# Performance work log

Measured on AMD Instinct MI355X. Metric: run time of the kernel, lower is better.

Reference implementation:

```python
import jax, jax.numpy as jnp
import numpy as np


def _dct_mats(N):
    # torch_dct.dct with norm=None: X_k = 2 * sum_n x_n cos(pi*(2n+1)k/(2N))
    # torch_dct.idct with norm=None is its exact inverse:
    #   x_n = (1/N) * (X_0/2 + sum_{k>=1} X_k cos(pi*(2n+1)k/(2N)))
    n = np.arange(N)
    k = np.arange(N)
    ang = np.pi * (2 * n[None, :] + 1) * k[:, None] / (2 * N)  # [k, n]
    cosang = np.cos(ang)
    D = (2.0 * cosang).astype(np.float32)                      # [k, n] DCT-II matrix
    scale = np.where(k == 0, 0.5, 1.0) / N                     # k=0 halved, /N overall
    Dinv = (cosang.T * scale[None, :]).astype(np.float32)      # [n, k] inverse matrix
    return jnp.asarray(D), jnp.asarray(Dinv)


def setup_inputs() -> dict:
    key = jax.random.key(0)
    k1, k2 = jax.random.split(key)
    B, C, H, W = 16, 28, 256, 256
    x = jax.random.normal(k1, (B, C, H, W), dtype=jnp.float32)
    weight = jax.random.normal(k2, (H, W, C), dtype=jnp.float32) * 0.02
    return {"x": x, "weight": weight}


def reference(x, weight):
    B, C, H, W = x.shape
    D, Dinv = _dct_mats(C)
    xt = jnp.transpose(x, (0, 2, 3, 1))            # [B, H, W, C]
    xd = jnp.einsum('bhwn,kn->bhwk', xt, D)        # DCT-II along channel dim
    xd = xd * weight                               # per-pixel spectral filter
    out = jnp.einsum('bhwk,nk->bhwn', xd, Dinv)    # inverse DCT along channel dim
    return jnp.transpose(out, (0, 3, 1, 2))        # back to [B, C, H, W]
```

## Files before the change

### kernel.cpp

```cpp
#include <hip/hip_runtime.h>

#define C_DIM 28
#define HW 65536
#define B_DIM 16

namespace {

constexpr double K_PI = 3.14159265358979323846;

constexpr double cos_taylor(double u) {
    double u2 = u * u;
    double term = 1.0, sum = 1.0;
    for (int i = 1; i <= 12; ++i) {
        term *= -u2 / (double)((2 * i - 1) * (2 * i));
        sum += term;
    }
    return sum;
}

constexpr double cos_pi_over56(int t) {
    t %= 112;
    if (t < 0) t += 112;
    double sign = 1.0;
    if (t > 56) t = 112 - t;
    if (t > 28) { t = 56 - t; sign = -1.0; }
    return sign * cos_taylor(K_PI * (double)t / 56.0);
}

struct Tables {
    float D[C_DIM][C_DIM];
    float Dinv[C_DIM][C_DIM];
};

constexpr Tables make_tables() {
    Tables t{};
    for (int k = 0; k < C_DIM; ++k) {
        for (int n = 0; n < C_DIM; ++n) {
            double c = cos_pi_over56((2 * n + 1) * k);
            t.D[k][n]    = (float)(2.0 * c);
            t.Dinv[n][k] = (float)(c * ((k == 0) ? 0.5 : 1.0) / (double)C_DIM);
        }
    }
    return t;
}

constexpr Tables TBL = make_tables();

}

__global__ __launch_bounds__(256) void spedct_kernel(
    const float* __restrict__ x,
    const float* __restrict__ w,
    float* __restrict__ out) {

    const int p  = blockIdx.x * 256 + threadIdx.x;
    const int b  = p >> 16;
    const int hw = p & 0xFFFF;

    const float* xp = x + (size_t)b * (C_DIM * HW) + hw;

    float xv[C_DIM];
#pragma unroll
    for (int n = 0; n < C_DIM; ++n) xv[n] = xp[(size_t)n * HW];

    float wv[C_DIM];
    const float4* wp = (const float4*)(w + (size_t)hw * C_DIM);
#pragma unroll
    for (int i = 0; i < 7; ++i) {
        float4 v = wp[i];
        wv[4 * i + 0] = v.x; wv[4 * i + 1] = v.y;
        wv[4 * i + 2] = v.z; wv[4 * i + 3] = v.w;
    }

    float xd[C_DIM];
#pragma unroll
    for (int k = 0; k < C_DIM; ++k) xd[k] = 0.0f;
#pragma unroll
    for (int n = 0; n < C_DIM; ++n) {
        const float xn = xv[n];
#pragma unroll
        for (int k = 0; k < C_DIM; ++k)
            xd[k] = fmaf(TBL.D[k][n], xn, xd[k]);
    }

#pragma unroll
    for (int k = 0; k < C_DIM; ++k) xd[k] *= wv[k];

    float o[C_DIM];
#pragma unroll
    for (int n = 0; n < C_DIM; ++n) o[n] = 0.0f;
#pragma unroll
    for (int k = 0; k < C_DIM; ++k) {
        const float xk = xd[k];
#pragma unroll
        for (int n = 0; n < C_DIM; ++n)
            o[n] = fmaf(TBL.Dinv[n][k], xk, o[n]);
    }

    float* op = out + (size_t)b * (C_DIM * HW) + hw;
#pragma unroll
    for (int n = 0; n < C_DIM; ++n) op[(size_t)n * HW] = o[n];
}

extern "C" void kernel_launch(void* const* d_in, const int* in_sizes, int n_in,
                              void* d_out, int out_size, void* d_ws, size_t ws_size,
                              hipStream_t stream) {
    const float* x = (const float*)d_in[0];
    const float* w = (const float*)d_in[1];
    float* out = (float*)d_out;

    const int total_pixels = B_DIM * HW;
    dim3 block(256);
    dim3 grid(total_pixels / 256);
    spedct_kernel<<<grid, block, 0, stream>>>(x, w, out);
}
```

Measured before the change: 215.6 us.

## Process four batches per thread with prefetch, weight reuse and nontemporal stores

Each thread now handles the same pixel across four batch items, loading the per-pixel weight row once and reusing it for all four. The next batch's 28 channel values are prefetched into a double buffer while the current one is computed. Output writes use nontemporal stores to avoid polluting cache. The grid shrinks to 1024 blocks, and the larger register footprint may lower occupancy.

```diff
diff --git a/kernel.cpp b/kernel.cpp
--- a/kernel.cpp
+++ b/kernel.cpp
@@ -3,6 +3,9 @@
 #define C_DIM 28
 #define HW 65536
 #define B_DIM 16
+#define ITER 4
+#define THREADS 256
+#define GRID 1024
 
 namespace {
 
@@ -53,53 +56,68 @@
     const float* __restrict__ w,
     float* __restrict__ out) {
 
-    const int p  = blockIdx.x * 256 + threadIdx.x;
-    const int b  = p >> 16;
-    const int hw = p & 0xFFFF;
-
-    const float* xp = x + (size_t)b * (C_DIM * HW) + hw;
-
-    float xv[C_DIM];
-#pragma unroll
-    for (int n = 0; n < C_DIM; ++n) xv[n] = xp[(size_t)n * HW];
+    const int t  = blockIdx.x * THREADS + threadIdx.x;
+    const int hw = t & (HW - 1);
+    const int b0 = t >> 16;
 
     float wv[C_DIM];
-    const float4* wp = (const float4*)(w + (size_t)hw * C_DIM);
+    const float4* wp4 = (const float4*)(w + (size_t)hw * C_DIM);
 #pragma unroll
     for (int i = 0; i < 7; ++i) {
-        float4 v = wp[i];
+        float4 v = wp4[i];
         wv[4 * i + 0] = v.x; wv[4 * i + 1] = v.y;
         wv[4 * i + 2] = v.z; wv[4 * i + 3] = v.w;
     }
 
-    float xd[C_DIM];
+    const size_t bstride = (size_t)ITER * C_DIM * HW;
+    const float* xp = x   + (size_t)b0 * C_DIM * HW + hw;
+    float*       op = out + (size_t)b0 * C_DIM * HW + hw;
+
+    float xv[2][C_DIM];
 #pragma unroll
-    for (int k = 0; k < C_DIM; ++k) xd[k] = 0.0f;
-#pragma unroll
-    for (int n = 0; n < C_DIM; ++n) {
-        const float xn = xv[n];
-#pragma unroll
-        for (int k = 0; k < C_DIM; ++k)
-            xd[k] = fmaf(TBL.D[k][n], xn, xd[k]);
-    }
+    for (int n = 0; n < C_DIM; ++n) xv[0][n] = xp[(size_t)n * HW];
 
 #pragma unroll
-    for (int k = 0; k < C_DIM; ++k) xd[k] *= wv[k];
+    for (int i = 0; i < ITER; ++i) {
+        if (i + 1 < ITER) {
+            const float* xn = xp + (size_t)(i + 1) * bstride;
+#pragma unroll
+            for (int n = 0; n < C_DIM; ++n)
+                xv[(i + 1) & 1][n] = xn[(size_t)n * HW];
+        }
 
-    float o[C_DIM];
+        const float* xc = xv[i & 1];
+
+        float xd[C_DIM];
 #pragma unroll
-    for (int n = 0; n < C_DIM; ++n) o[n] = 0.0f;
+        for (int k = 0; k < C_DIM; ++k) xd[k] = TBL.D[k][0] * xc[0];
 #pragma unroll
-    for (int k = 0; k < C_DIM; ++k) {
-        const float xk = xd[k];
+        for (int n = 1; n < C_DIM; ++n) {
+            const float xn_ = xc[n];
+#pragma unroll
+            for (int k = 0; k < C_DIM; ++k)
+                xd[k] = fmaf(TBL.D[k][n], xn_, xd[k]);
+        }
+
+#pragma unroll
+        for (int k = 0; k < C_DIM; ++k) xd[k] *= wv[k];
+
+        float o[C_DIM];
+#pragma unroll
+        for (int n = 0; n < C_DIM; ++n) o[n] = TBL.Dinv[n][0] * xd[0];
+#pragma unroll
+        for (int k = 1; k < C_DIM; ++k) {
+            const float xk = xd[k];
+#pragma unroll
+            for (int n = 0; n < C_DIM; ++n)
+                o[n] = fmaf(TBL.Dinv[n][k], xk, o[n]);
+        }
+
+        float* oo = op + (size_t)i * bstride;
 #pragma unroll
         for (int n = 0; n < C_DIM; ++n)
-            o[n] = fmaf(TBL.Dinv[n][k], xk, o[n]);
+            __builtin_nontemporal_store(o[n], &oo[(size_t)n * HW]);
     }
-
-    float* op = out + (size_t)b * (C_DIM * HW) + hw;
-#pragma unroll
-    for (int n = 0; n < C_DIM; ++n) op[(size_t)n * HW] = o[n];
 }
 
 extern "C" void kernel_launch(void* const* d_in, const int* in_sizes, int n_in,
@@ -109,8 +127,5 @@
     const float* w = (const float*)d_in[1];
     float* out = (float*)d_out;
 
-    const int total_pixels = B_DIM * HW;
-    dim3 block(256);
-    dim3 grid(total_pixels / 256);
-    spedct_kernel<<<grid, block, 0, stream>>>(x, w, out);
+    spedct_kernel<<<dim3(GRID), dim3(THREADS), 0, stream>>>(x, w, out);
 }
```

Result: no change. 214.2 us (-0.7%).

## Exploit DCT even/odd symmetry to halve channel-mixing FMAs

Applied to the files above, without the earlier changes.

Splits the 28-point DCT and inverse DCT into even/odd halves using the symmetry of the cosine matrix. Each transform then needs two 14x14 products after a butterfly instead of one 28x28 product, roughly halving the FMA count. The change also adds a launch-bounds occupancy hint and switches output writes to nontemporal stores. The kernel is largely memory-bound, so the arithmetic saving may matter less than the store and occupancy changes.

```diff
diff --git a/kernel.cpp b/kernel.cpp
--- a/kernel.cpp
+++ b/kernel.cpp
@@ -1,8 +1,10 @@
 #include <hip/hip_runtime.h>
 
 #define C_DIM 28
+#define HALF 14
 #define HW 65536
-#define B_DIM 16
+#define THREADS 256
+#define GRID 4096
 
 namespace {
 
@@ -28,19 +30,25 @@
 }
 
 struct Tables {
-    float D[C_DIM][C_DIM];
-    float Dinv[C_DIM][C_DIM];
+    float De[HALF][HALF], Do[HALF][HALF];
+    float Ge[HALF][HALF], Go[HALF][HALF];
 };
 
 constexpr Tables make_tables() {
     Tables t{};
-    for (int k = 0; k < C_DIM; ++k) {
-        for (int n = 0; n < C_DIM; ++n) {
-            double c = cos_pi_over56((2 * n + 1) * k);
-            t.D[k][n]    = (float)(2.0 * c);
-            t.Dinv[n][k] = (float)(c * ((k == 0) ? 0.5 : 1.0) / (double)C_DIM);
+    for (int m = 0; m < HALF; ++m)
+        for (int j = 0; j < HALF; ++j) {
+            t.De[m][j] = (float)(2.0 * cos_pi_over56((2 * j + 1) * (2 * m)));
+            t.Do[m][j] = (float)(2.0 * cos_pi_over56((2 * j + 1) * (2 * m + 1)));
         }
-    }
+    for (int n = 0; n < HALF; ++n)
+        for (int m = 0; m < HALF; ++m) {
+            int ke = 2 * m, ko = 2 * m + 1;
+            double se = ((ke == 0) ? 0.5 : 1.0) / (double)C_DIM;
+            double so = 1.0 / (double)C_DIM;
+            t.Ge[n][m] = (float)(cos_pi_over56((2 * n + 1) * ke) * se);
+            t.Go[n][m] = (float)(cos_pi_over56((2 * n + 1) * ko) * so);
+        }
     return t;
 }
 
@@ -48,14 +56,14 @@
 
 }
 
-__global__ __launch_bounds__(256) void spedct_kernel(
+__global__ __launch_bounds__(256, 4) void spedct_kernel(
     const float* __restrict__ x,
     const float* __restrict__ w,
     float* __restrict__ out) {
 
-    const int p  = blockIdx.x * 256 + threadIdx.x;
+    const int p  = blockIdx.x * THREADS + threadIdx.x;
     const int b  = p >> 16;
-    const int hw = p & 0xFFFF;
+    const int hw = p & (HW - 1);
 
     const float* xp = x + (size_t)b * (C_DIM * HW) + hw;
 
@@ -64,42 +72,65 @@
     for (int n = 0; n < C_DIM; ++n) xv[n] = xp[(size_t)n * HW];
 
     float wv[C_DIM];
-    const float4* wp = (const float4*)(w + (size_t)hw * C_DIM);
+    const float4* wp4 = (const float4*)(w + (size_t)hw * C_DIM);
 #pragma unroll
     for (int i = 0; i < 7; ++i) {
-        float4 v = wp[i];
+        float4 v = wp4[i];
         wv[4 * i + 0] = v.x; wv[4 * i + 1] = v.y;
         wv[4 * i + 2] = v.z; wv[4 * i + 3] = v.w;
     }
 
-    float xd[C_DIM];
+    float e[HALF], f[HALF];
 #pragma unroll
-    for (int k = 0; k < C_DIM; ++k) xd[k] = 0.0f;
+    for (int j = 0; j < HALF; ++j) {
+        e[j] = xv[j] + xv[27 - j];
+        f[j] = xv[j] - xv[27 - j];
+    }
+
+    float ye[HALF], yo[HALF];
 #pragma unroll
-    for (int n = 0; n < C_DIM; ++n) {
-        const float xn = xv[n];
+    for (int m = 0; m < HALF; ++m) {
+        ye[m] = TBL.De[m][0] * e[0];
+        yo[m] = TBL.Do[m][0] * f[0];
+    }
 #pragma unroll
-        for (int k = 0; k < C_DIM; ++k)
-            xd[k] = fmaf(TBL.D[k][n], xn, xd[k]);
+    for (int j = 1; j < HALF; ++j) {
+        const float ej = e[j], fj = f[j];
+#pragma unroll
+        for (int m = 0; m < HALF; ++m) {
+            ye[m] = fmaf(TBL.De[m][j], ej, ye[m]);
+            yo[m] = fmaf(TBL.Do[m][j], fj, yo[m]);
+        }
     }
 
 #pragma unroll
-    for (int k = 0; k < C_DIM; ++k) xd[k] *= wv[k];
+    for (int m = 0; m < HALF; ++m) {
+        ye[m] *= wv[2 * m];
+        yo[m] *= wv[2 * m + 1];
+    }
 
-    float o[C_DIM];
+    float E[HALF], O[HALF];
 #pragma unroll
-    for (int n = 0; n < C_DIM; ++n) o[n] = 0.0f;
+    for (int n = 0; n < HALF; ++n) {
+        E[n] = TBL.Ge[n][0] * ye[0];
+        O[n] = TBL.Go[n][0] * yo[0];
+    }
 #pragma unroll
-    for (int k = 0; k < C_DIM; ++k) {
-        const float xk = xd[k];
+    for (int m = 1; m < HALF; ++m) {
+        const float ym = ye[m], zm = yo[m];
 #pragma unroll
-        for (int n = 0; n < C_DIM; ++n)
-            o[n] = fmaf(TBL.Dinv[n][k], xk, o[n]);
+        for (int n = 0; n < HALF; ++n) {
+            E[n] = fmaf(TBL.Ge[n][m], ym, E[n]);
+            O[n] = fmaf(TBL.Go[n][m], zm, O[n]);
+        }
     }
 
     float* op = out + (size_t)b * (C_DIM * HW) + hw;
 #pragma unroll
-    for (int n = 0; n < C_DIM; ++n) op[(size_t)n * HW] = o[n];
+    for (int n = 0; n < HALF; ++n) {
+        __builtin_nontemporal_store(E[n] + O[n], &op[(size_t)n * HW]);
+        __builtin_nontemporal_store(E[n] - O[n], &op[(size_t)(27 - n) * HW]);
+    }
 }
 
 extern "C" void kernel_launch(void* const* d_in, const int* in_sizes, int n_in,
@@ -109,8 +140,5 @@
     const float* w = (const float*)d_in[1];
     float* out = (float*)d_out;
 
-    const int total_pixels = B_DIM * HW;
-    dim3 block(256);
-    dim3 grid(total_pixels / 256);
-    spedct_kernel<<<grid, block, 0, stream>>>(x, w, out);
+    spedct_kernel<<<dim3(GRID), dim3(THREADS), 0, stream>>>(x, w, out);
 }
```

Result: no change. 215.2 us (-0.2%).
